# Performance work log

Hardware: AMD Instinct MI355X
Metric: run time of the kernel (lower is better)

## Reference

```python
import jax, jax.numpy as jnp
import numpy as np

B, V, D = 2048, 3129, 768  # batch, answer vocab, BERT embed dim


def setup_inputs() -> dict:
    key = jax.random.key(0)
    k1, k2, k3, k4 = jax.random.split(key, 4)
    prediction = jax.random.normal(k1, (B, V), dtype=jnp.float32)
    # sparse multi-label soft scores: ~10 nonzero answers per row (VQA-style)
    soft = jax.random.uniform(k2, (B, V), dtype=jnp.float32)
    keep = jax.random.uniform(k3, (B, V)) < 0.003
    label = jnp.where(keep, soft, 0.0)
    Embedding = jax.random.normal(k4, (V, D), dtype=jnp.float32)
    return {"prediction": prediction, "label": label, "Embedding": Embedding}


def reference(prediction, label, Embedding):
    V_ = Embedding.shape[0]
    # cosine-style normalization of the Gram matrix (row norms of sim itself,
    # exactly as in the torch code)
    sim = Embedding @ Embedding.T                              # [V, V]
    n = jnp.sqrt((sim ** 2).sum(1, keepdims=True))             # [V, 1]
    sim = sim / (n @ n.T + 1e-8)
    sim = jnp.where(jnp.eye(V_, dtype=bool), -2.0, sim)        # mask diagonal
    mapping = jnp.argmax(sim, axis=1)                          # [V] int

    # vectorized replacement of the per-batch/per-nonzero python loop:
    # semantic_a[i, mapping[g]] = label[i, g] for every nonzero label[i, g].
    # entries with label==0 are routed to out-of-bounds index V and dropped.
    Bn = label.shape[0]
    idx = jnp.where(label != 0, mapping[None, :], V_)          # [B, V]
    rows = jnp.arange(Bn)[:, None]                             # [B, 1]
    semantic_a = jnp.zeros_like(label).at[rows, idx].set(label, mode="drop")

    # BCE-with-logits, mean reduction, scaled by labels.size(1)
    bce = jnp.logaddexp(0.0, prediction) - prediction * semantic_a
    return jnp.mean(bce) * V_
```

## Files before the change

kernel.cpp:

```cpp
#include <hip/hip_runtime.h>
#include <hip/hip_bf16.h>

#define VN 3129
#define DN 768
#define BN 2048
#define NT 3200
#define NB64 50
#define NTRI64 1275

typedef __attribute__((ext_vector_type(8))) short bf16x8;
typedef __attribute__((ext_vector_type(4))) float f32x4;

typedef __attribute__((address_space(3))) void as3_void;
typedef __attribute__((address_space(1))) const void as1_cvoid;

__device__ __forceinline__ void gload16(const void* g, void* l) {
    __builtin_amdgcn_global_load_lds((as1_cvoid*)g, (as3_void*)l, 16, 0, 0);
}

__device__ __forceinline__ unsigned sortable_f32(float f) {
    unsigned u = __float_as_uint(f);
    return (u & 0x80000000u) ? ~u : (u | 0x80000000u);
}

__device__ __forceinline__ int xcd_swz(int orig) {
    const int q = NTRI64 / 8, r = NTRI64 % 8;
    int xcd = orig & 7, idx = orig >> 3;
    return (xcd < r ? xcd * (q + 1) : r * (q + 1) + (xcd - r) * q) + idx;
}

static const size_t WB_EB  = 0;
static const size_t WB_SIM = 4915200;
static const size_t WB_N2  = 15360000;
static const size_t WB_ARG = 15372800;
static const size_t WB_P1  = 15385600;
static const size_t WB_P2  = 15393792;
static const size_t WB_GSL = 15401984;
static const size_t WB_LSL = 15926272;
static const size_t WB_CNT = 16450560;
static const size_t WS_NEEDED = 16458752;
static const int GRID_PREP = 2048;

__global__ __launch_bounds__(256) void k_prep(const float* __restrict__ E,
                                              const float* __restrict__ pred,
                                              const float* __restrict__ label,
                                              unsigned short* __restrict__ Eb,
                                              unsigned* __restrict__ zwords,
                                              float* __restrict__ part1,
                                              unsigned* __restrict__ gsl,
                                              float* __restrict__ lsl,
                                              unsigned* __restrict__ cntarr) {
    const int tid = threadIdx.x;
    const int gid = blockIdx.x * 256 + tid;
    const int gstride = gridDim.x * 256;
    const int lane = tid & 63;

    for (int i = gid; i < 6400; i += gstride) zwords[i] = 0u;

    const int nchunks = NT * DN / 8;
    for (int chunk = gid; chunk < nchunks; chunk += gstride) {
        int row = chunk / (DN / 8);
        int cc = (chunk % (DN / 8)) * 8;
        unsigned short o[8];
        if (row < VN) {
            const float* src = E + (size_t)row * DN + cc;
            float4 a = *(const float4*)src;
            float4 b = *(const float4*)(src + 4);
            float v[8] = {a.x, a.y, a.z, a.w, b.x, b.y, b.z, b.w};
#pragma unroll
            for (int t = 0; t < 8; ++t) {
                unsigned u = __float_as_uint(v[t]);
                u += 0x7FFFu + ((u >> 16) & 1u);
                o[t] = (unsigned short)(u >> 16);
            }
        } else {
#pragma unroll
            for (int t = 0; t < 8; ++t) o[t] = 0;
        }
        *(uint4*)(Eb + (size_t)chunk * 8) = *(const uint4*)o;
    }

    {
        const float4* p4 = (const float4*)pred;
        const int n4 = BN * VN / 4;
        float acc = 0.f;
        for (int i = gid; i < n4; i += gstride) {
            float4 v = p4[i];
            acc += fmaxf(v.x, 0.f) + __logf(1.f + __expf(-fabsf(v.x)));
            acc += fmaxf(v.y, 0.f) + __logf(1.f + __expf(-fabsf(v.y)));
            acc += fmaxf(v.z, 0.f) + __logf(1.f + __expf(-fabsf(v.z)));
            acc += fmaxf(v.w, 0.f) + __logf(1.f + __expf(-fabsf(v.w)));
        }
        for (int off = 32; off; off >>= 1) acc += __shfl_down(acc, off);
        __shared__ float wsum[4];
        int wid = tid >> 6;
        if (lane == 0) wsum[wid] = acc;
        __syncthreads();
        if (tid == 0) part1[blockIdx.x] = wsum[0] + wsum[1] + wsum[2] + wsum[3];
    }

    {
        const int wave_gid = gid >> 6;
        if (wave_gid < BN) {
            const int row = wave_gid;
            const float* lrow = label + (size_t)row * VN;
            float4 buf[12];
#pragma unroll
            for (int c = 0; c < 12; ++c)
                buf[c] = *(const float4*)(lrow + c * 256 + lane * 4);
            float tailv = 0.f;
            const int gtail = 3072 + lane;
            if (lane < VN - 3072) tailv = lrow[gtail];

            int base = 0;
#pragma unroll
            for (int c = 0; c < 12; ++c) {
                const float* f = (const float*)&buf[c];
#pragma unroll
                for (int e = 0; e < 4; ++e) {
                    float l = f[e];
                    unsigned long long mask = __ballot(l != 0.f);
                    if (l != 0.f) {
                        int pos = base + __popcll(mask & ((1ull << lane) - 1ull));
                        if (pos < 64) {
                            gsl[row * 64 + pos] = (unsigned)(c * 256 + lane * 4 + e);
                            lsl[row * 64 + pos] = l;
                        }
                    }
                    base += __popcll(mask);
                }
            }
            {
                unsigned long long mask = __ballot(tailv != 0.f);
                if (tailv != 0.f) {
                    int pos = base + __popcll(mask & ((1ull << lane) - 1ull));
                    if (pos < 64) {
                        gsl[row * 64 + pos] = (unsigned)gtail;
                        lsl[row * 64 + pos] = tailv;
                    }
                }
                base += __popcll(mask);
            }
            if (lane == 0) cntarr[row] = (unsigned)base;
        }
    }
}

__global__ __launch_bounds__(256) void k_gram64s(const unsigned short* __restrict__ Eb,
                                                 float* __restrict__ n2,
                                                 unsigned short* __restrict__ simT) {
    __shared__ __align__(16) unsigned short As[64 * 64];
    __shared__ __align__(16) unsigned short Bs[64 * 64];
    const int tid = threadIdx.x;
    const int lane = tid & 63;
    const int w = tid >> 6;
    const int wr = w >> 1, wc = w & 1;

    int t = xcd_swz(blockIdx.x), bi = 0, rem = t;
    while (rem >= NB64 - bi) { rem -= NB64 - bi; ++bi; }
    const int bj = bi + rem;
    const int i0 = bi * 64, j0 = bj * 64;

    const int srow = lane >> 3;
    const int scol = 8 * ((lane & 7) ^ (lane >> 3));

    f32x4 acc[2][2] = {};

    for (int k0 = 0; k0 < DN; k0 += 64) {
#pragma unroll
        for (int q = 0; q < 2; ++q) {
            int ci = w * 2 + q;
            int row = ci * 8 + srow;
            gload16(Eb + (size_t)(i0 + row) * DN + k0 + scol, As + ci * 512);
            gload16(Eb + (size_t)(j0 + row) * DN + k0 + scol, Bs + ci * 512);
        }
        __syncthreads();
        const int rA = wr * 32 + (lane & 15);
        const int rB = wc * 32 + (lane & 15);
        const int swr = (lane & 7) << 4;
        const int kb = (lane >> 4) * 16;
#pragma unroll
        for (int ks = 0; ks < 2; ++ks) {
            const int cb = (kb + ks * 64) ^ swr;
            bf16x8 af[2], bfr[2];
#pragma unroll
            for (int m = 0; m < 2; ++m)
                af[m] = *(const bf16x8*)((const char*)As + (rA + m * 16) * 128 + cb);
#pragma unroll
            for (int n = 0; n < 2; ++n)
                bfr[n] = *(const bf16x8*)((const char*)Bs + (rB + n * 16) * 128 + cb);
#pragma unroll
            for (int m = 0; m < 2; ++m)
#pragma unroll
                for (int n = 0; n < 2; ++n)
                    acc[m][n] = __builtin_amdgcn_mfma_f32_16x16x32_bf16(
                        af[m], bfr[n], acc[m][n], 0, 0, 0);
        }
        __syncthreads();
    }

    const int rr4 = (lane >> 4) * 4;

    {
        unsigned op[8];
#pragma unroll
        for (int m = 0; m < 2; ++m)
#pragma unroll
            for (int n = 0; n < 2; ++n)
#pragma unroll
                for (int ih = 0; ih < 2; ++ih) {
                    unsigned lo = __float_as_uint(acc[m][n][ih * 2]);
                    lo += 0x7FFFu + ((lo >> 16) & 1u);
                    unsigned hi = __float_as_uint(acc[m][n][ih * 2 + 1]);
                    hi += 0x7FFFu + ((hi >> 16) & 1u);
                    op[(m * 2 + n) * 2 + ih] = (lo >> 16) | (hi & 0xFFFF0000u);
                }
        uint4* dst = (uint4*)(simT + (size_t)t * 4096 + (size_t)tid * 16);
        dst[0] = *(uint4*)&op[0];
        dst[1] = *(uint4*)&op[4];
    }

    __shared__ float red[64];
    if (tid < 64) red[tid] = 0.f;
    __syncthreads();
#pragma unroll
    for (int m = 0; m < 2; ++m)
#pragma unroll
        for (int i = 0; i < 4; ++i) {
            float s = acc[m][0][i] * acc[m][0][i] + acc[m][1][i] * acc[m][1][i];
            s += __shfl_xor(s, 1); s += __shfl_xor(s, 2);
            s += __shfl_xor(s, 4); s += __shfl_xor(s, 8);
            if ((lane & 15) == 0)
                atomicAdd(&red[wr * 32 + m * 16 + rr4 + i], s);
        }
    __syncthreads();
    if (tid < 64) atomicAdd(&n2[i0 + tid], red[tid]);
    if (bi != bj) {
        __syncthreads();
        if (tid < 64) red[tid] = 0.f;
        __syncthreads();
#pragma unroll
        for (int n = 0; n < 2; ++n) {
            float s = 0.f;
#pragma unroll
            for (int m = 0; m < 2; ++m)
#pragma unroll
                for (int i = 0; i < 4; ++i) { float x = acc[m][n][i]; s += x * x; }
            s += __shfl_xor(s, 16); s += __shfl_xor(s, 32);
            if (lane < 16)
                atomicAdd(&red[wc * 32 + n * 16 + lane], s);
        }
        __syncthreads();
        if (tid < 64) atomicAdd(&n2[j0 + tid], red[tid]);
    }
}

__global__ __launch_bounds__(256) void k_amax64(const unsigned short* __restrict__ simT,
                                                const float* __restrict__ n2,
                                                unsigned* __restrict__ argbest) {
    const int tid = threadIdx.x, lane = tid & 63, w = tid >> 6;
    const int wr = w >> 1, wc = w & 1;
    int t = xcd_swz(blockIdx.x), bi = 0, rem = t;
    while (rem >= NB64 - bi) { rem -= NB64 - bi; ++bi; }
    const int bj = bi + rem;
    const int i0 = bi * 64, j0 = bj * 64;

    __shared__ float rni_s[64], rnj_s[64];
    __shared__ unsigned rbest[64], cbest[64];
    if (tid < 64) {
        rni_s[tid] = rsqrtf(n2[i0 + tid]);
        rnj_s[tid] = rsqrtf(n2[j0 + tid]);
        rbest[tid] = 0u; cbest[tid] = 0u;
    }
    __syncthreads();

    const uint4* src = (const uint4*)(simT + (size_t)t * 4096 + (size_t)tid * 16);
    uint4 iv0 = src[0], iv1 = src[1];
    unsigned ip[8];
    *(uint4*)&ip[0] = iv0; *(uint4*)&ip[4] = iv1;

    const int rr4 = (lane >> 4) * 4;
    int rg[8]; float rni8[8];
#pragma unroll
    for (int m = 0; m < 2; ++m)
#pragma unroll
        for (int i = 0; i < 4; ++i) {
            int rl = wr * 32 + m * 16 + rr4 + i;
            rg[m * 4 + i] = i0 + rl;
            rni8[m * 4 + i] = rni_s[rl];
        }
    int cg2[2]; float rnj2[2];
#pragma unroll
    for (int n = 0; n < 2; ++n) {
        int cl = wc * 32 + n * 16 + (lane & 15);
        cg2[n] = j0 + cl;
        rnj2[n] = rnj_s[cl];
    }

#pragma unroll
    for (int m = 0; m < 2; ++m)
#pragma unroll
        for (int i = 0; i < 4; ++i) {
            int ig = rg[m * 4 + i];
            unsigned best = 0u;
#pragma unroll
            for (int n = 0; n < 2; ++n) {
                int jg = cg2[n];
                if (jg < VN && jg != ig) {
                    unsigned wv = ip[(m * 2 + n) * 2 + (i >> 1)];
                    float v = __uint_as_float((i & 1) ? (wv & 0xFFFF0000u) : (wv << 16));
                    unsigned key = (sortable_f32(v * rnj2[n]) & 0xFFFFF000u) | (unsigned)jg;
                    best = max(best, key);
                }
            }
            best = max(best, __shfl_xor(best, 1));
            best = max(best, __shfl_xor(best, 2));
            best = max(best, __shfl_xor(best, 4));
            best = max(best, __shfl_xor(best, 8));
            if ((lane & 15) == 0)
                atomicMax(&rbest[wr * 32 + m * 16 + rr4 + i], best);
        }

    if (bi != bj) {
#pragma unroll
        for (int n = 0; n < 2; ++n) {
            unsigned best = 0u;
#pragma unroll
            for (int m = 0; m < 2; ++m)
#pragma unroll
                for (int i = 0; i < 4; ++i) {
                    int ig = rg[m * 4 + i];
                    if (ig < VN) {
                        unsigned wv = ip[(m * 2 + n) * 2 + (i >> 1)];
                        float v = __uint_as_float((i & 1) ? (wv & 0xFFFF0000u) : (wv << 16));
                        unsigned key = (sortable_f32(v * rni8[m * 4 + i]) & 0xFFFFF000u)
                                       | (unsigned)ig;
                        best = max(best, key);
                    }
                }
            best = max(best, __shfl_xor(best, 16));
            best = max(best, __shfl_xor(best, 32));
            if (lane < 16)
                atomicMax(&cbest[wc * 32 + n * 16 + lane], best);
        }
    }
    __syncthreads();
    if (tid < 64) {
        unsigned rb = rbest[tid];
        if (rb) atomicMax(&argbest[i0 + tid], rb);
        if (bi != bj) {
            unsigned cb = cbest[tid];
            if (cb) atomicMax(&argbest[j0 + tid], cb);
        }
    }
}

__global__ __launch_bounds__(64) void k_scatter(const float* __restrict__ pred,
                                                const float* __restrict__ label,
                                                const unsigned* __restrict__ argbest,
                                                const unsigned* __restrict__ gsl,
                                                const float* __restrict__ lsl,
                                                const unsigned* __restrict__ cntarr,
                                                float* __restrict__ part2) {
    const int i = blockIdx.x;
    const int lane = threadIdx.x;
    const int cnt = (int)cntarr[i];
    float contrib = 0.f;

    if (cnt <= 64) {
        unsigned g = 0, tgt = 0xFFFFFFFFu;
        float l = 0.f;
        if (lane < cnt) {
            g = gsl[i * 64 + lane];
            l = lsl[i * 64 + lane];
            tgt = argbest[g] & 0xFFFu;
        }
        __shared__ unsigned tg_s[64], g_s[64];
        tg_s[lane] = tgt; g_s[lane] = g;
        __syncthreads();
        if (lane < cnt) {
            bool keep = true;
            for (int o = 0; o < cnt; ++o)
                if (tg_s[o] == tgt && g_s[o] > g) { keep = false; break; }
            if (keep) contrib = pred[(size_t)i * VN + tgt] * l;
        }
    } else {
        __shared__ int c2;
        __shared__ unsigned short gs2[256], ts2[256];
        __shared__ float ls2[256];
        if (lane == 0) c2 = 0;
        __syncthreads();
        const float* lrow = label + (size_t)i * VN;
        for (int g = lane; g < VN; g += 64) {
            float l = lrow[g];
            if (l != 0.f) {
                int p = atomicAdd(&c2, 1);
                if (p < 256) {
                    gs2[p] = (unsigned short)g;
                    ls2[p] = l;
                    ts2[p] = (unsigned short)(argbest[g] & 0xFFFu);
                }
            }
        }
        __syncthreads();
        int m = min(c2, 256);
        for (int e = lane; e < m; e += 64) {
            bool keep = true;
            for (int o = 0; o < m; ++o)
                if (ts2[o] == ts2[e] && gs2[o] > gs2[e]) keep = false;
            if (keep) contrib += pred[(size_t)i * VN + ts2[e]] * ls2[e];
        }
    }

    for (int off = 32; off; off >>= 1) contrib += __shfl_down(contrib, off);
    if (lane == 0) part2[i] = contrib;
}

__global__ __launch_bounds__(256) void k_final(const float* __restrict__ part1, int p1n,
                                               const float* __restrict__ part2,
                                               float* __restrict__ out) {
    int tid = threadIdx.x;
    double acc = 0.0;
    for (int i = tid; i < p1n; i += 256) acc += (double)part1[i];
    for (int i = tid; i < BN; i += 256) acc -= (double)part2[i];
    __shared__ double red[256];
    red[tid] = acc;
    __syncthreads();
    for (int s = 128; s; s >>= 1) {
        if (tid < s) red[tid] += red[tid + s];
        __syncthreads();
    }
    if (tid == 0) out[0] = (float)(red[0] / (double)BN);
}

__global__ __launch_bounds__(256) void k_zero(unsigned int* p, int nwords) {
    int idx = blockIdx.x * 256 + threadIdx.x;
    for (int i = idx; i < nwords; i += gridDim.x * 256) p[i] = 0u;
}

__global__ __launch_bounds__(256) void k_logexp(const float* __restrict__ pred,
                                                float* __restrict__ part1) {
    int tid = threadIdx.x;
    const float4* p4 = (const float4*)pred;
    const int n4 = BN * VN / 4;
    float acc = 0.f;
    for (int i = blockIdx.x * 256 + tid; i < n4; i += gridDim.x * 256) {
        float4 v = p4[i];
        acc += fmaxf(v.x, 0.f) + log1pf(__expf(-fabsf(v.x)));
        acc += fmaxf(v.y, 0.f) + log1pf(__expf(-fabsf(v.y)));
        acc += fmaxf(v.z, 0.f) + log1pf(__expf(-fabsf(v.z)));
        acc += fmaxf(v.w, 0.f) + log1pf(__expf(-fabsf(v.w)));
    }
    for (int off = 32; off; off >>= 1) acc += __shfl_down(acc, off);
    __shared__ float wsum[4];
    int lane = tid & 63, wid = tid >> 6;
    if (lane == 0) wsum[wid] = acc;
    __syncthreads();
    if (tid == 0) part1[blockIdx.x] = wsum[0] + wsum[1] + wsum[2] + wsum[3];
}

template <int PASS>
__global__ __launch_bounds__(256) void k_gemm(const float* __restrict__ E,
                                              float* __restrict__ n2,
                                              unsigned* __restrict__ argbest) {
    __shared__ float As[16][132];
    __shared__ float Bs[16][132];
    const int tid = threadIdx.x;
    const int tx = tid & 15, ty = tid >> 4;
    const int i0 = blockIdx.y * 128, j0 = blockIdx.x * 128;
    float acc[8][8] = {};

    for (int k0 = 0; k0 < DN; k0 += 16) {
#pragma unroll
        for (int h = 0; h < 2; ++h) {
            int f = tid + h * 256;
            int r = f >> 2;
            int kq = (f & 3) << 2;
            int gi = i0 + r;
            float4 va = make_float4(0.f, 0.f, 0.f, 0.f);
            if (gi < VN) va = *(const float4*)(E + gi * DN + k0 + kq);
            As[kq + 0][r] = va.x; As[kq + 1][r] = va.y;
            As[kq + 2][r] = va.z; As[kq + 3][r] = va.w;
            int gj = j0 + r;
            float4 vb = make_float4(0.f, 0.f, 0.f, 0.f);
            if (gj < VN) vb = *(const float4*)(E + gj * DN + k0 + kq);
            Bs[kq + 0][r] = vb.x; Bs[kq + 1][r] = vb.y;
            Bs[kq + 2][r] = vb.z; Bs[kq + 3][r] = vb.w;
        }
        __syncthreads();
#pragma unroll
        for (int k = 0; k < 16; ++k) {
            float a[8], b[8];
            *(float4*)&a[0] = *(const float4*)&As[k][ty * 8];
            *(float4*)&a[4] = *(const float4*)&As[k][ty * 8 + 4];
            *(float4*)&b[0] = *(const float4*)&Bs[k][tx * 8];
            *(float4*)&b[4] = *(const float4*)&Bs[k][tx * 8 + 4];
#pragma unroll
            for (int m = 0; m < 8; ++m)
#pragma unroll
                for (int n = 0; n < 8; ++n)
                    acc[m][n] = fmaf(a[m], b[n], acc[m][n]);
        }
        __syncthreads();
    }

    if (PASS == 0) {
        __shared__ float nrow[128];
        if (tid < 128) nrow[tid] = 0.f;
        __syncthreads();
#pragma unroll
        for (int m = 0; m < 8; ++m) {
            float s = 0.f;
#pragma unroll
            for (int n = 0; n < 8; ++n) s += acc[m][n] * acc[m][n];
            atomicAdd(&nrow[ty * 8 + m], s);
        }
        __syncthreads();
        if (tid < 128 && i0 + tid < VN) atomicAdd(&n2[i0 + tid], nrow[tid]);
    } else {
        __shared__ unsigned brow[128];
        if (tid < 128) brow[tid] = 0u;
        __syncthreads();
        float rnj[8];
#pragma unroll
        for (int n = 0; n < 8; ++n) {
            int j = j0 + tx * 8 + n;
            rnj[n] = (j < VN) ? rsqrtf(n2[j]) : 0.f;
        }
#pragma unroll
        for (int m = 0; m < 8; ++m) {
            int i = i0 + ty * 8 + m;
            unsigned best = 0u;
#pragma unroll
            for (int n = 0; n < 8; ++n) {
                int j = j0 + tx * 8 + n;
                if (j < VN && j != i) {
                    unsigned key = (sortable_f32(acc[m][n] * rnj[n]) & 0xFFFFF000u) | (unsigned)j;
                    best = max(best, key);
                }
            }
            atomicMax(&brow[ty * 8 + m], best);
        }
        __syncthreads();
        if (tid < 128 && i0 + tid < VN) atomicMax(&argbest[i0 + tid], brow[tid]);
    }
}

__global__ __launch_bounds__(256) void k_scatter_scan(const float* __restrict__ pred,
                                                      const float* __restrict__ label,
                                                      const unsigned* __restrict__ argbest,
                                                      float* __restrict__ part2) {
    int i = blockIdx.x;
    int tid = threadIdx.x;
    __shared__ int cnt;
    __shared__ unsigned short gs[256];
    __shared__ unsigned short ts[256];
    __shared__ float ls[256];
    if (tid == 0) cnt = 0;
    __syncthreads();
    const float* lrow = label + (size_t)i * VN;
    for (int g = tid; g < VN; g += 256) {
        float l = lrow[g];
        if (l != 0.f) {
            int p = atomicAdd(&cnt, 1);
            if (p < 256) {
                gs[p] = (unsigned short)g;
                ls[p] = l;
                ts[p] = (unsigned short)(argbest[g] & 0xFFFu);
            }
        }
    }
    __syncthreads();
    int m = min(cnt, 256);
    float contrib = 0.f;
    for (int e = tid; e < m; e += 256) {
        bool keep = true;
        for (int o = 0; o < m; ++o)
            if (ts[o] == ts[e] && gs[o] > gs[e]) keep = false;
        if (keep) contrib += pred[(size_t)i * VN + ts[e]] * ls[e];
    }
    for (int off = 32; off; off >>= 1) contrib += __shfl_down(contrib, off);
    __shared__ float wsum[4];
    int lane = tid & 63, wid = tid >> 6;
    if (lane == 0) wsum[wid] = contrib;
    __syncthreads();
    if (tid == 0) part2[i] = wsum[0] + wsum[1] + wsum[2] + wsum[3];
}

extern "C" void kernel_launch(void* const* d_in, const int* in_sizes, int n_in,
                              void* d_out, int out_size, void* d_ws, size_t ws_size,
                              hipStream_t stream) {
    (void)in_sizes; (void)n_in; (void)out_size;
    const float* pred  = (const float*)d_in[0];
    const float* label = (const float*)d_in[1];
    const float* E     = (const float*)d_in[2];
    float* out = (float*)d_out;
    char* wsb = (char*)d_ws;

    if (ws_size >= WS_NEEDED) {
        unsigned short* Eb   = (unsigned short*)(wsb + WB_EB);
        unsigned short* simT = (unsigned short*)(wsb + WB_SIM);
        float* n2    = (float*)(wsb + WB_N2);
        unsigned* argbest = (unsigned*)(wsb + WB_ARG);
        float* part1 = (float*)(wsb + WB_P1);
        float* part2 = (float*)(wsb + WB_P2);
        unsigned* gsl = (unsigned*)(wsb + WB_GSL);
        float* lsl   = (float*)(wsb + WB_LSL);
        unsigned* cntarr = (unsigned*)(wsb + WB_CNT);

        k_prep<<<GRID_PREP, 256, 0, stream>>>(E, pred, label, Eb, (unsigned*)n2,
                                              part1, gsl, lsl, cntarr);
        k_gram64s<<<NTRI64, 256, 0, stream>>>(Eb, n2, simT);
        k_amax64<<<NTRI64, 256, 0, stream>>>(simT, n2, argbest);
        k_scatter<<<BN, 64, 0, stream>>>(pred, label, argbest, gsl, lsl, cntarr, part2);
        k_final<<<1, 256, 0, stream>>>(part1, GRID_PREP, part2, out);
    } else {
        float* ws = (float*)d_ws;
        float* n2    = ws;
        unsigned* argbest = (unsigned*)(ws + 3200);
        float* part1 = ws + 6400;
        float* part2 = ws + 8448;
        k_zero<<<10, 256, 0, stream>>>((unsigned int*)ws, 6400);
        k_logexp<<<2048, 256, 0, stream>>>(pred, part1);
        dim3 g((VN + 127) / 128, (VN + 127) / 128);
        k_gemm<0><<<g, 256, 0, stream>>>(E, n2, argbest);
        k_gemm<1><<<g, 256, 0, stream>>>(E, n2, argbest);
        k_scatter_scan<<<BN, 256, 0, stream>>>(pred, label, argbest, part2);
        k_final<<<1, 256, 0, stream>>>(part1, 2048, part2, out);
    }
}
```

Baseline: 54.38 us.

## Move softplus reduction into gram kernel and label compaction into argmax kernel

Splits the heavy prep kernel so it only converts the embedding to bf16 and zeroes accumulators. The softplus sum over predictions is folded into the Gram GEMM kernel, which prefetches its prediction slice into registers before the matmul and reduces it at the end. Label nonzero compaction moves into the argmax kernel, with label rows loaded at kernel start. The aim is to hide these memory-bound passes behind compute-bound kernels and shorten the serial prep stage, at the cost of extra register pressure that may lower occupancy of the GEMM and argmax kernels.

```diff
diff --git a/kernel.cpp b/kernel.cpp
--- a/kernel.cpp
+++ b/kernel.cpp
@@ -39,21 +39,12 @@
 static const size_t WB_LSL = 15926272;
 static const size_t WB_CNT = 16450560;
 static const size_t WS_NEEDED = 16458752;
-static const int GRID_PREP = 2048;
-
-__global__ __launch_bounds__(256) void k_prep(const float* __restrict__ E,
-                                              const float* __restrict__ pred,
-                                              const float* __restrict__ label,
-                                              unsigned short* __restrict__ Eb,
-                                              unsigned* __restrict__ zwords,
-                                              float* __restrict__ part1,
-                                              unsigned* __restrict__ gsl,
-                                              float* __restrict__ lsl,
-                                              unsigned* __restrict__ cntarr) {
-    const int tid = threadIdx.x;
-    const int gid = blockIdx.x * 256 + tid;
+
+__global__ __launch_bounds__(256) void k_prep2(const float* __restrict__ E,
+                                               unsigned short* __restrict__ Eb,
+                                               unsigned* __restrict__ zwords) {
+    const int gid = blockIdx.x * 256 + threadIdx.x;
     const int gstride = gridDim.x * 256;
-    const int lane = tid & 63;
 
     for (int i = gid; i < 6400; i += gstride) zwords[i] = 0u;
 
@@ -79,82 +70,29 @@
         }
         *(uint4*)(Eb + (size_t)chunk * 8) = *(const uint4*)o;
     }
-
-    {
-        const float4* p4 = (const float4*)pred;
-        const int n4 = BN * VN / 4;
-        float acc = 0.f;
-        for (int i = gid; i < n4; i += gstride) {
-            float4 v = p4[i];
-            acc += fmaxf(v.x, 0.f) + __logf(1.f + __expf(-fabsf(v.x)));
-            acc += fmaxf(v.y, 0.f) + __logf(1.f + __expf(-fabsf(v.y)));
-            acc += fmaxf(v.z, 0.f) + __logf(1.f + __expf(-fabsf(v.z)));
-            acc += fmaxf(v.w, 0.f) + __logf(1.f + __expf(-fabsf(v.w)));
-        }
-        for (int off = 32; off; off >>= 1) acc += __shfl_down(acc, off);
-        __shared__ float wsum[4];
-        int wid = tid >> 6;
-        if (lane == 0) wsum[wid] = acc;
-        __syncthreads();
-        if (tid == 0) part1[blockIdx.x] = wsum[0] + wsum[1] + wsum[2] + wsum[3];
-    }
-
-    {
-        const int wave_gid = gid >> 6;
-        if (wave_gid < BN) {
-            const int row = wave_gid;
-            const float* lrow = label + (size_t)row * VN;
-            float4 buf[12];
-#pragma unroll
-            for (int c = 0; c < 12; ++c)
-                buf[c] = *(const float4*)(lrow + c * 256 + lane * 4);
-            float tailv = 0.f;
-            const int gtail = 3072 + lane;
-            if (lane < VN - 3072) tailv = lrow[gtail];
-
-            int base = 0;
-#pragma unroll
-            for (int c = 0; c < 12; ++c) {
-                const float* f = (const float*)&buf[c];
-#pragma unroll
-                for (int e = 0; e < 4; ++e) {
-                    float l = f[e];
-                    unsigned long long mask = __ballot(l != 0.f);
-                    if (l != 0.f) {
-                        int pos = base + __popcll(mask & ((1ull << lane) - 1ull));
-                        if (pos < 64) {
-                            gsl[row * 64 + pos] = (unsigned)(c * 256 + lane * 4 + e);
-                            lsl[row * 64 + pos] = l;
-                        }
-                    }
-                    base += __popcll(mask);
-                }
-            }
-            {
-                unsigned long long mask = __ballot(tailv != 0.f);
-                if (tailv != 0.f) {
-                    int pos = base + __popcll(mask & ((1ull << lane) - 1ull));
-                    if (pos < 64) {
-                        gsl[row * 64 + pos] = (unsigned)gtail;
-                        lsl[row * 64 + pos] = tailv;
-                    }
-                }
-                base += __popcll(mask);
-            }
-            if (lane == 0) cntarr[row] = (unsigned)base;
-        }
-    }
 }
 
 __global__ __launch_bounds__(256) void k_gram64s(const unsigned short* __restrict__ Eb,
+                                                 const float* __restrict__ pred,
                                                  float* __restrict__ n2,
-                                                 unsigned short* __restrict__ simT) {
+                                                 unsigned short* __restrict__ simT,
+                                                 float* __restrict__ part1) {
     __shared__ __align__(16) unsigned short As[64 * 64];
     __shared__ __align__(16) unsigned short Bs[64 * 64];
     const int tid = threadIdx.x;
     const int lane = tid & 63;
     const int w = tid >> 6;
     const int wr = w >> 1, wc = w & 1;
+
+    const int n4 = BN * VN / 4;
+    const int pbase = blockIdx.x * 256 + tid;
+    float4 pv[5];
+#pragma unroll
+    for (int k = 0; k < 5; ++k) {
+        int idx = pbase + k * (NTRI64 * 256);
+        pv[k] = make_float4(0.f, 0.f, 0.f, 0.f);
+        if (idx < n4) pv[k] = ((const float4*)pred)[idx];
+    }
 
     int t = xcd_swz(blockIdx.x), bi = 0, rem = t;
     while (rem >= NB64 - bi) { rem -= NB64 - bi; ++bi; }
@@ -253,13 +191,51 @@
         __syncthreads();
         if (tid < 64) atomicAdd(&n2[j0 + tid], red[tid]);
     }
+
+    {
+        float alx = 0.f;
+#pragma unroll
+        for (int k = 0; k < 5; ++k) {
+            if (pbase + k * (NTRI64 * 256) < n4) {
+                float4 v = pv[k];
+                alx += fmaxf(v.x, 0.f) + __logf(1.f + __expf(-fabsf(v.x)));
+                alx += fmaxf(v.y, 0.f) + __logf(1.f + __expf(-fabsf(v.y)));
+                alx += fmaxf(v.z, 0.f) + __logf(1.f + __expf(-fabsf(v.z)));
+                alx += fmaxf(v.w, 0.f) + __logf(1.f + __expf(-fabsf(v.w)));
+            }
+        }
+        for (int off = 32; off; off >>= 1) alx += __shfl_down(alx, off);
+        __syncthreads();
+        if (lane == 0) red[w] = alx;
+        __syncthreads();
+        if (tid == 0) part1[blockIdx.x] = red[0] + red[1] + red[2] + red[3];
+    }
 }
 
 __global__ __launch_bounds__(256) void k_amax64(const unsigned short* __restrict__ simT,
+                                                const float* __restrict__ label,
                                                 const float* __restrict__ n2,
-                                                unsigned* __restrict__ argbest) {
+                                                unsigned* __restrict__ argbest,
+                                                unsigned* __restrict__ gsl,
+                                                float* __restrict__ lsl,
+                                                unsigned* __restrict__ cntarr) {
     const int tid = threadIdx.x, lane = tid & 63, w = tid >> 6;
     const int wr = w >> 1, wc = w & 1;
+
+    const int lrow_id = blockIdx.x * 4 + w;
+    float4 lbuf[12];
+    float tailv = 0.f;
+    if (lrow_id < BN) {
+        const float* lrow = label + (size_t)lrow_id * VN;
+#pragma unroll
+        for (int c = 0; c < 12; ++c)
+            lbuf[c] = *(const float4*)(lrow + c * 256 + lane * 4);
+        if (lane < VN - 3072) tailv = lrow[3072 + lane];
+    } else {
+#pragma unroll
+        for (int c = 0; c < 12; ++c) lbuf[c] = make_float4(0.f, 0.f, 0.f, 0.f);
+    }
+
     int t = xcd_swz(blockIdx.x), bi = 0, rem = t;
     while (rem >= NB64 - bi) { rem -= NB64 - bi; ++bi; }
     const int bj = bi + rem;
@@ -353,6 +329,39 @@
             if (cb) atomicMax(&argbest[j0 + tid], cb);
         }
     }
+
+    if (lrow_id < BN) {
+        int base = 0;
+#pragma unroll
+        for (int c = 0; c < 12; ++c) {
+            const float* f = (const float*)&lbuf[c];
+#pragma unroll
+            for (int e = 0; e < 4; ++e) {
+                float l = f[e];
+                unsigned long long mask = __ballot(l != 0.f);
+                if (l != 0.f) {
+                    int pos = base + __popcll(mask & ((1ull << lane) - 1ull));
+                    if (pos < 64) {
+                        gsl[lrow_id * 64 + pos] = (unsigned)(c * 256 + lane * 4 + e);
+                        lsl[lrow_id * 64 + pos] = l;
+                    }
+                }
+                base += __popcll(mask);
+            }
+        }
+        {
+            unsigned long long mask = __ballot(tailv != 0.f);
+            if (tailv != 0.f) {
+                int pos = base + __popcll(mask & ((1ull << lane) - 1ull));
+                if (pos < 64) {
+                    gsl[lrow_id * 64 + pos] = (unsigned)(3072 + lane);
+                    lsl[lrow_id * 64 + pos] = tailv;
+                }
+            }
+            base += __popcll(mask);
+        }
+        if (lane == 0) cntarr[lrow_id] = (unsigned)base;
+    }
 }
 
 __global__ __launch_bounds__(64) void k_scatter(const float* __restrict__ pred,
@@ -608,12 +617,11 @@
         float* lsl   = (float*)(wsb + WB_LSL);
         unsigned* cntarr = (unsigned*)(wsb + WB_CNT);
 
-        k_prep<<<GRID_PREP, 256, 0, stream>>>(E, pred, label, Eb, (unsigned*)n2,
-                                              part1, gsl, lsl, cntarr);
-        k_gram64s<<<NTRI64, 256, 0, stream>>>(Eb, n2, simT);
-        k_amax64<<<NTRI64, 256, 0, stream>>>(simT, n2, argbest);
+        k_prep2<<<1024, 256, 0, stream>>>(E, Eb, (unsigned*)n2);
+        k_gram64s<<<NTRI64, 256, 0, stream>>>(Eb, pred, n2, simT, part1);
+        k_amax64<<<NTRI64, 256, 0, stream>>>(simT, label, n2, argbest, gsl, lsl, cntarr);
         k_scatter<<<BN, 64, 0, stream>>>(pred, label, argbest, gsl, lsl, cntarr, part2);
-        k_final<<<1, 256, 0, stream>>>(part1, GRID_PREP, part2, out);
+        k_final<<<1, 256, 0, stream>>>(part1, NTRI64, part2, out);
     } else {
         float* ws = (float*)d_ws;
         float* n2    = ws;
```

Measured after the change: 54.73 us. About the same (+0.7%).

## Merge Gram GEMM with logexp and label compaction into one heterogeneous kernel

Applied to the files above, without the earlier changes.

Splits the old prep kernel so only the bf16 conversion and zeroing stay in a first kernel. The Gram tile GEMM, softplus reduction and label compaction then run as separate block ranges of one combined launch. This lets the bandwidth-bound prediction and label passes overlap with the MFMA-bound Gram tiles instead of serialising them. It adds shared-memory pressure from the union of block roles and may change occupancy for the GEMM blocks.

```diff
diff --git a/kernel.cpp b/kernel.cpp
--- a/kernel.cpp
+++ b/kernel.cpp
@@ -7,6 +7,9 @@
 #define NT 3200
 #define NB64 50
 #define NTRI64 1275
+#define NBLK_LOGEXP 512
+#define NBLK_COMPACT 512
+#define GRID_MEGA (NTRI64 + NBLK_LOGEXP + NBLK_COMPACT)
 
 typedef __attribute__((ext_vector_type(8))) short bf16x8;
 typedef __attribute__((ext_vector_type(4))) float f32x4;
@@ -39,21 +42,12 @@
 static const size_t WB_LSL = 15926272;
 static const size_t WB_CNT = 16450560;
 static const size_t WS_NEEDED = 16458752;
-static const int GRID_PREP = 2048;
-
-__global__ __launch_bounds__(256) void k_prep(const float* __restrict__ E,
-                                              const float* __restrict__ pred,
-                                              const float* __restrict__ label,
-                                              unsigned short* __restrict__ Eb,
-                                              unsigned* __restrict__ zwords,
-                                              float* __restrict__ part1,
-                                              unsigned* __restrict__ gsl,
-                                              float* __restrict__ lsl,
-                                              unsigned* __restrict__ cntarr) {
-    const int tid = threadIdx.x;
-    const int gid = blockIdx.x * 256 + tid;
+
+__global__ __launch_bounds__(256) void k_prep2(const float* __restrict__ E,
+                                               unsigned short* __restrict__ Eb,
+                                               unsigned* __restrict__ zwords) {
+    const int gid = blockIdx.x * 256 + threadIdx.x;
     const int gstride = gridDim.x * 256;
-    const int lane = tid & 63;
 
     for (int i = gid; i < 6400; i += gstride) zwords[i] = 0u;
 
@@ -79,12 +73,130 @@
         }
         *(uint4*)(Eb + (size_t)chunk * 8) = *(const uint4*)o;
     }
-
-    {
+}
+
+__global__ __launch_bounds__(256) void k_mega(const unsigned short* __restrict__ Eb,
+                                              const float* __restrict__ pred,
+                                              const float* __restrict__ label,
+                                              float* __restrict__ n2,
+                                              unsigned short* __restrict__ simT,
+                                              float* __restrict__ part1,
+                                              unsigned* __restrict__ gsl,
+                                              float* __restrict__ lsl,
+                                              unsigned* __restrict__ cntarr) {
+    const int bid = blockIdx.x;
+    const int tid = threadIdx.x;
+    const int lane = tid & 63;
+    const int w = tid >> 6;
+
+    if (bid < NTRI64) {
+        __shared__ __align__(16) unsigned short As[64 * 64];
+        __shared__ __align__(16) unsigned short Bs[64 * 64];
+        const int wr = w >> 1, wc = w & 1;
+
+        int t = xcd_swz(bid), bi = 0, rem = t;
+        while (rem >= NB64 - bi) { rem -= NB64 - bi; ++bi; }
+        const int bj = bi + rem;
+        const int i0 = bi * 64, j0 = bj * 64;
+
+        const int srow = lane >> 3;
+        const int scol = 8 * ((lane & 7) ^ (lane >> 3));
+
+        f32x4 acc[2][2] = {};
+
+        for (int k0 = 0; k0 < DN; k0 += 64) {
+#pragma unroll
+            for (int q = 0; q < 2; ++q) {
+                int ci = w * 2 + q;
+                int row = ci * 8 + srow;
+                gload16(Eb + (size_t)(i0 + row) * DN + k0 + scol, As + ci * 512);
+                gload16(Eb + (size_t)(j0 + row) * DN + k0 + scol, Bs + ci * 512);
+            }
+            __syncthreads();
+            const int rA = wr * 32 + (lane & 15);
+            const int rB = wc * 32 + (lane & 15);
+            const int swr = (lane & 7) << 4;
+            const int kb = (lane >> 4) * 16;
+#pragma unroll
+            for (int ks = 0; ks < 2; ++ks) {
+                const int cb = (kb + ks * 64) ^ swr;
+                bf16x8 af[2], bfr[2];
+#pragma unroll
+                for (int m = 0; m < 2; ++m)
+                    af[m] = *(const bf16x8*)((const char*)As + (rA + m * 16) * 128 + cb);
+#pragma unroll
+                for (int n = 0; n < 2; ++n)
+                    bfr[n] = *(const bf16x8*)((const char*)Bs + (rB + n * 16) * 128 + cb);
+#pragma unroll
+                for (int m = 0; m < 2; ++m)
+#pragma unroll
+                    for (int n = 0; n < 2; ++n)
+                        acc[m][n] = __builtin_amdgcn_mfma_f32_16x16x32_bf16(
+                            af[m], bfr[n], acc[m][n], 0, 0, 0);
+            }
+            __syncthreads();
+        }
+
+        const int rr4 = (lane >> 4) * 4;
+
+        {
+            unsigned op[8];
+#pragma unroll
+            for (int m = 0; m < 2; ++m)
+#pragma unroll
+                for (int n = 0; n < 2; ++n)
+#pragma unroll
+                    for (int ih = 0; ih < 2; ++ih) {
+                        unsigned lo = __float_as_uint(acc[m][n][ih * 2]);
+                        lo += 0x7FFFu + ((lo >> 16) & 1u);
+                        unsigned hi = __float_as_uint(acc[m][n][ih * 2 + 1]);
+                        hi += 0x7FFFu + ((hi >> 16) & 1u);
+                        op[(m * 2 + n) * 2 + ih] = (lo >> 16) | (hi & 0xFFFF0000u);
+                    }
+            uint4* dst = (uint4*)(simT + (size_t)t * 4096 + (size_t)tid * 16);
+            dst[0] = *(uint4*)&op[0];
+            dst[1] = *(uint4*)&op[4];
+        }
+
+        __shared__ float red[64];
+        if (tid < 64) red[tid] = 0.f;
+        __syncthreads();
+#pragma unroll
+        for (int m = 0; m < 2; ++m)
+#pragma unroll
+            for (int i = 0; i < 4; ++i) {
+                float s = acc[m][0][i] * acc[m][0][i] + acc[m][1][i] * acc[m][1][i];
+                s += __shfl_xor(s, 1); s += __shfl_xor(s, 2);
+                s += __shfl_xor(s, 4); s += __shfl_xor(s, 8);
+                if ((lane & 15) == 0)
+                    atomicAdd(&red[wr * 32 + m * 16 + rr4 + i], s);
+            }
+        __syncthreads();
+        if (tid < 64) atomicAdd(&n2[i0 + tid], red[tid]);
+        if (bi != bj) {
+            __syncthreads();
+            if (tid < 64) red[tid] = 0.f;
+            __syncthreads();
+#pragma unroll
+            for (int n = 0; n < 2; ++n) {
+                float s = 0.f;
+#pragma unroll
+                for (int m = 0; m < 2; ++m)
+#pragma unroll
+                    for (int i = 0; i < 4; ++i) { float x = acc[m][n][i]; s += x * x; }
+                s += __shfl_xor(s, 16); s += __shfl_xor(s, 32);
+                if (lane < 16)
+                    atomicAdd(&red[wc * 32 + n * 16 + lane], s);
+            }
+            __syncthreads();
+            if (tid < 64) atomicAdd(&n2[j0 + tid], red[tid]);
+        }
+    } else if (bid < NTRI64 + NBLK_LOGEXP) {
+        const int rb = bid - NTRI64;
         const float4* p4 = (const float4*)pred;
         const int n4 = BN * VN / 4;
         float acc = 0.f;
-        for (int i = gid; i < n4; i += gstride) {
+        for (int i = rb * 256 + tid; i < n4; i += NBLK_LOGEXP * 256) {
             float4 v = p4[i];
             acc += fmaxf(v.x, 0.f) + __logf(1.f + __expf(-fabsf(v.x)));
             acc += fmaxf(v.y, 0.f) + __logf(1.f + __expf(-fabsf(v.y)));
@@ -93,16 +205,12 @@
         }
         for (int off = 32; off; off >>= 1) acc += __shfl_down(acc, off);
         __shared__ float wsum[4];
-        int wid = tid >> 6;
-        if (lane == 0) wsum[wid] = acc;
-        __syncthreads();
-        if (tid == 0) part1[blockIdx.x] = wsum[0] + wsum[1] + wsum[2] + wsum[3];
-    }
-
-    {
-        const int wave_gid = gid >> 6;
-        if (wave_gid < BN) {
-            const int row = wave_gid;
+        if (lane == 0) wsum[w] = acc;
+        __syncthreads();
+        if (tid == 0) part1[rb] = wsum[0] + wsum[1] + wsum[2] + wsum[3];
+    } else {
+        const int row = (bid - NTRI64 - NBLK_LOGEXP) * 4 + w;
+        if (row < BN) {
             const float* lrow = label + (size_t)row * VN;
             float4 buf[12];
 #pragma unroll
@@ -143,115 +251,6 @@
             }
             if (lane == 0) cntarr[row] = (unsigned)base;
         }
-    }
-}
-
-__global__ __launch_bounds__(256) void k_gram64s(const unsigned short* __restrict__ Eb,
-                                                 float* __restrict__ n2,
-                                                 unsigned short* __restrict__ simT) {
-    __shared__ __align__(16) unsigned short As[64 * 64];
-    __shared__ __align__(16) unsigned short Bs[64 * 64];
-    const int tid = threadIdx.x;
-    const int lane = tid & 63;
-    const int w = tid >> 6;
-    const int wr = w >> 1, wc = w & 1;
-
-    int t = xcd_swz(blockIdx.x), bi = 0, rem = t;
-    while (rem >= NB64 - bi) { rem -= NB64 - bi; ++bi; }
-    const int bj = bi + rem;
-    const int i0 = bi * 64, j0 = bj * 64;
-
-    const int srow = lane >> 3;
-    const int scol = 8 * ((lane & 7) ^ (lane >> 3));
-
-    f32x4 acc[2][2] = {};
-
-    for (int k0 = 0; k0 < DN; k0 += 64) {
-#pragma unroll
-        for (int q = 0; q < 2; ++q) {
-            int ci = w * 2 + q;
-            int row = ci * 8 + srow;
-            gload16(Eb + (size_t)(i0 + row) * DN + k0 + scol, As + ci * 512);
-            gload16(Eb + (size_t)(j0 + row) * DN + k0 + scol, Bs + ci * 512);
-        }
-        __syncthreads();
-        const int rA = wr * 32 + (lane & 15);
-        const int rB = wc * 32 + (lane & 15);
-        const int swr = (lane & 7) << 4;
-        const int kb = (lane >> 4) * 16;
-#pragma unroll
-        for (int ks = 0; ks < 2; ++ks) {
-            const int cb = (kb + ks * 64) ^ swr;
-            bf16x8 af[2], bfr[2];
-#pragma unroll
-            for (int m = 0; m < 2; ++m)
-                af[m] = *(const bf16x8*)((const char*)As + (rA + m * 16) * 128 + cb);
-#pragma unroll
-            for (int n = 0; n < 2; ++n)
-                bfr[n] = *(const bf16x8*)((const char*)Bs + (rB + n * 16) * 128 + cb);
-#pragma unroll
-            for (int m = 0; m < 2; ++m)
-#pragma unroll
-                for (int n = 0; n < 2; ++n)
-                    acc[m][n] = __builtin_amdgcn_mfma_f32_16x16x32_bf16(
-                        af[m], bfr[n], acc[m][n], 0, 0, 0);
-        }
-        __syncthreads();
-    }
-
-    const int rr4 = (lane >> 4) * 4;
-
-    {
-        unsigned op[8];
-#pragma unroll
-        for (int m = 0; m < 2; ++m)
-#pragma unroll
-            for (int n = 0; n < 2; ++n)
-#pragma unroll
-                for (int ih = 0; ih < 2; ++ih) {
-                    unsigned lo = __float_as_uint(acc[m][n][ih * 2]);
-                    lo += 0x7FFFu + ((lo >> 16) & 1u);
-                    unsigned hi = __float_as_uint(acc[m][n][ih * 2 + 1]);
-                    hi += 0x7FFFu + ((hi >> 16) & 1u);
-                    op[(m * 2 + n) * 2 + ih] = (lo >> 16) | (hi & 0xFFFF0000u);
-                }
-        uint4* dst = (uint4*)(simT + (size_t)t * 4096 + (size_t)tid * 16);
-        dst[0] = *(uint4*)&op[0];
-        dst[1] = *(uint4*)&op[4];
-    }
-
-    __shared__ float red[64];
-    if (tid < 64) red[tid] = 0.f;
-    __syncthreads();
-#pragma unroll
-    for (int m = 0; m < 2; ++m)
-#pragma unroll
-        for (int i = 0; i < 4; ++i) {
-            float s = acc[m][0][i] * acc[m][0][i] + acc[m][1][i] * acc[m][1][i];
-            s += __shfl_xor(s, 1); s += __shfl_xor(s, 2);
-            s += __shfl_xor(s, 4); s += __shfl_xor(s, 8);
-            if ((lane & 15) == 0)
-                atomicAdd(&red[wr * 32 + m * 16 + rr4 + i], s);
-        }
-    __syncthreads();
-    if (tid < 64) atomicAdd(&n2[i0 + tid], red[tid]);
-    if (bi != bj) {
-        __syncthreads();
-        if (tid < 64) red[tid] = 0.f;
-        __syncthreads();
-#pragma unroll
-        for (int n = 0; n < 2; ++n) {
-            float s = 0.f;
-#pragma unroll
-            for (int m = 0; m < 2; ++m)
-#pragma unroll
-                for (int i = 0; i < 4; ++i) { float x = acc[m][n][i]; s += x * x; }
-            s += __shfl_xor(s, 16); s += __shfl_xor(s, 32);
-            if (lane < 16)
-                atomicAdd(&red[wc * 32 + n * 16 + lane], s);
-        }
-        __syncthreads();
-        if (tid < 64) atomicAdd(&n2[j0 + tid], red[tid]);
     }
 }
 
@@ -608,12 +607,12 @@
         float* lsl   = (float*)(wsb + WB_LSL);
         unsigned* cntarr = (unsigned*)(wsb + WB_CNT);
 
-        k_prep<<<GRID_PREP, 256, 0, stream>>>(E, pred, label, Eb, (unsigned*)n2,
+        k_prep2<<<1024, 256, 0, stream>>>(E, Eb, (unsigned*)n2);
+        k_mega<<<GRID_MEGA, 256, 0, stream>>>(Eb, pred, label, n2, simT,
                                               part1, gsl, lsl, cntarr);
-        k_gram64s<<<NTRI64, 256, 0, stream>>>(Eb, n2, simT);
         k_amax64<<<NTRI64, 256, 0, stream>>>(simT, n2, argbest);
         k_scatter<<<BN, 64, 0, stream>>>(pred, label, argbest, gsl, lsl, cntarr, part2);
-        k_final<<<1, 256, 0, stream>>>(part1, GRID_PREP, part2, out);
+        k_final<<<1, 256, 0, stream>>>(part1, NBLK_LOGEXP, part2, out);
     } else {
         float* ws = (float*)d_ws;
         float* n2    = ws;
```

Result: faster. 52.60 us (-3.3%).
